# Optimization experiments

Hardware: AMD Instinct MI355X
Metric: run time of the kernel (lower is better)

The kernel has to match this reference:

```python
import jax, jax.numpy as jnp
import numpy as np

B, S, NH, D_IN = 64, 512, 4, 256   # batch, seq_len, rnn n_head, input_dim
H = 256                            # hidden_dim == attention activation_dim
AH = 256                           # attention_hidden_dim (attn out_dim)
OUT = 3                            # output_dim (sentiment classes)


def setup_inputs() -> dict:
    key = jax.random.key(0)
    ks = jax.random.split(key, 9)
    def p(k, shape, scale=0.05):
        return jax.random.normal(k, shape, dtype=jnp.float32) * scale
    return dict(
        x=jax.random.normal(ks[0], (B, S, NH, D_IN), dtype=jnp.float32),
        Wk=p(ks[1], (D_IN, H)), bk=jnp.zeros((H,), jnp.float32),
        Wq=p(ks[2], (H, H)),    bq=jnp.zeros((H,), jnp.float32),
        w_mlp=p(ks[3], (2 * H,)),
        Wproj=p(ks[4], (H, AH)), bproj=jnp.zeros((AH,), jnp.float32),
        W1=p(ks[5], (D_IN + AH, H)), b1=jnp.zeros((H,), jnp.float32),
        W2=p(ks[6], (H, H)),    b2=jnp.zeros((H,), jnp.float32),
        Wo=p(ks[7], (NH * H, OUT)), bo=jnp.zeros((OUT,), jnp.float32),
    )


def _cell(x_t, hidden, params):
    Wk, bk, Wq, bq, w_mlp, Wproj, bproj, W1, b1, W2, b2, Wo, bo = params
    kx = x_t @ Wk + bk           # [B, NH, H]  keys from step input
    qx = hidden @ Wq + bq        # [B, NH, H]  queries from hidden state
    w1, w2 = w_mlp[:H], w_mlp[H:]
    # MLP score: s[b,i,j] = tanh(cat(kx[b,j], qx[b,i]) . w) = tanh(kx[b,j].w1 + qx[b,i].w2)
    score = jnp.tanh((qx @ w2)[:, :, None] + (kx @ w1)[:, None, :])  # [B, NH, NH]
    score = jax.nn.softmax(score, axis=-1)
    attn = jnp.einsum('bij,bjh->bih', score, kx) @ Wproj + bproj     # [B, NH, AH]
    concat = jnp.concatenate([x_t, attn], axis=-1)                   # [B, NH, D_IN+AH]
    hidden_new = jax.nn.relu(concat @ W1 + b1) @ W2 + b2             # [B, NH, H]
    logits = hidden_new.reshape(B, NH * H) @ Wo + bo                 # [B, OUT]
    out = jax.nn.log_softmax(logits, axis=-1)
    return out, hidden_new


def reference(x, Wk, bk, Wq, bq, w_mlp, Wproj, bproj, W1, b1, W2, b2, Wo, bo):
    params = (Wk, bk, Wq, bq, w_mlp, Wproj, bproj, W1, b1, W2, b2, Wo, bo)
    h0 = jnp.zeros((B, NH, H), x.dtype)
    xs = jnp.swapaxes(x, 0, 1)  # [S, B, NH, D_IN] for scan over time
    def step(h, x_t):
        out, h_new = _cell(x_t, h, params)
        return h_new, out
    h_final, outs = jax.lax.scan(step, h0, xs)
    # return_sequence=False: last-step log-softmax output and final hidden
    return outs[-1], h_final
```

## Files before the change

kernel.cpp:

```cpp
#include <hip/hip_runtime.h>
#include <hip/hip_bf16.h>
#include <math.h>

#define BB   64
#define SS   512
#define NHH  4
#define DD   256
#define HH   256
#define LDH  264

typedef __attribute__((ext_vector_type(8))) short  short8;
typedef __attribute__((ext_vector_type(4))) float  floatx4;


__device__ __forceinline__ unsigned short f2b(float f) {
  __hip_bfloat16 h = __float2bfloat16(f);
  return __builtin_bit_cast(unsigned short, h);
}
__device__ __forceinline__ float b2f(unsigned short u) {
  unsigned v = (unsigned)u << 16;
  return __builtin_bit_cast(float, v);
}

__global__ __launch_bounds__(256) void init1_kernel(
    const float* __restrict__ Wk, const float* __restrict__ Wproj,
    const float* __restrict__ W1, const float* __restrict__ Wq,
    const float* __restrict__ bq, const float* __restrict__ w_mlp,
    const float* __restrict__ W2, const float* __restrict__ b2,
    const float* __restrict__ bk,
    float* __restrict__ ws, unsigned short* __restrict__ wpack)
{
  __shared__ float vsh[256];
  __shared__ float red[256];
  int tid = threadIdx.x;
  int b = blockIdx.x;

  if (b == 0) {
    const float* w2 = w_mlp + HH;
    {
      float a = 0.f;
      const float4* Wq4 = (const float4*)(Wq + tid * 256);
      const float4* w24 = (const float4*)w2;
      for (int k = 0; k < 64; ++k) {
        float4 wv = Wq4[k], xv = w24[k];
        a = fmaf(wv.x, xv.x, fmaf(wv.y, xv.y, fmaf(wv.z, xv.z, fmaf(wv.w, xv.w, a))));
      }
      vsh[tid] = a;
    }
    __syncthreads();
    {
      float a2 = 0.f;
      const float4* W24 = (const float4*)(W2 + tid * 256);
      const float4* v4  = (const float4*)vsh;
      for (int k = 0; k < 64; ++k) {
        float4 wv = W24[k], xv = v4[k];
        a2 = fmaf(wv.x, xv.x, fmaf(wv.y, xv.y, fmaf(wv.z, xv.z, fmaf(wv.w, xv.w, a2))));
      }
      ws[tid] = 2.f * a2;
    }
    red[tid] = bq[tid] * w_mlp[HH + tid];
    __syncthreads();
    for (int s = 128; s; s >>= 1) { if (tid < s) red[tid] += red[tid + s]; __syncthreads(); }
    float c = red[0];
    __syncthreads();
    ws[768 + tid] = 2.f * c;
    red[tid] = b2[tid] * vsh[tid];
    __syncthreads();
    for (int s = 128; s; s >>= 1) { if (tid < s) red[tid] += red[tid + s]; __syncthreads(); }
    if (tid == 0) ws[512] = 2.f * (red[0] + c);
    __syncthreads();
    red[tid] = bk[tid] * w_mlp[tid];
    __syncthreads();
    for (int s = 128; s; s >>= 1) { if (tid < s) red[tid] += red[tid + s]; __syncthreads(); }
    if (tid == 0) ws[513] = 2.f * red[0];
    return;
  }

  if (b <= 256) {
    int idx = (b - 1) * 256 + tid;
    int j    = idx & 7;
    int lane = (idx >> 3) & 63;
    int ks   = (idx >> 9) & 7;
    int pan  = idx >> 12;
    int k = ks * 32 + ((lane >> 4) << 3) + j;
    int n = pan * 16 + (lane & 15);
    wpack[idx] = f2b(W1[k * 256 + n]);
    return;
  }

  {
    int r = b - 257;
    const float* w1b = W1 + 256 * 256;
    float acc = 0.f;
    for (int k = 0; k < 256; ++k)
      acc = fmaf(Wproj[r * 256 + k], w1b[k * 256 + tid], acc);
    ws[132096 + r * 256 + tid] = acc;
  }
}

__global__ __launch_bounds__(256) void init2_kernel(
    const float* __restrict__ Wk, const float* __restrict__ W1,
    const float* __restrict__ bproj, const float* __restrict__ bk,
    const float* __restrict__ w_mlp, const float* __restrict__ b1,
    float* __restrict__ ws, unsigned short* __restrict__ wpack)
{
  __shared__ float red[256];
  int tid = threadIdx.x;
  int b = blockIdx.x;
  const float* Wc = ws + 132096;

  if (b < 256) {
    int r = b;
    float acc = 0.f;
    for (int k = 0; k < 256; ++k)
      acc = fmaf(Wk[r * 256 + k], Wc[k * 256 + tid], acc);
    int n = tid;
    int pan = n >> 4, ks = r >> 5, j = r & 7;
    int lane = ((r >> 3) & 3) * 16 + (n & 15);
    wpack[65536 + pan * 4096 + ks * 512 + lane * 8 + j] = f2b(acc);
    red[tid] = Wk[r * 256 + tid] * w_mlp[tid];
    __syncthreads();
    for (int s = 128; s; s >>= 1) { if (tid < s) red[tid] += red[tid + s]; __syncthreads(); }
    if (tid == 0) ws[197632 + r] = 2.f * red[0];
    return;
  }

  {
    const float* w1b = W1 + 256 * 256;
    float a3 = 0.f;
    for (int k = 0; k < 256; ++k)
      a3 = fmaf(bproj[k], w1b[k * 256 + tid], a3);
    for (int k = 0; k < 256; ++k)
      a3 = fmaf(bk[k], Wc[k * 256 + tid], a3);
    ws[256 + tid] = a3;
    ws[197888 + tid] = a3 + b1[tid];
  }
}

__device__ __forceinline__ void mfma_gemm4(
    const unsigned short* A_lds, const short8* __restrict__ Bp,
    const float* __restrict__ bias, floatx4 acc[4][4], int l, int w)
{
  int col = l & 15, quad = l >> 4;
#pragma unroll
  for (int pp = 0; pp < 4; ++pp) {
    float bv = bias ? bias[(w * 4 + pp) * 16 + col] : 0.f;
#pragma unroll
    for (int mf = 0; mf < 4; ++mf)
      acc[mf][pp] = (floatx4){bv, bv, bv, bv};
  }
  const short8* Bb = Bp + (size_t)(w * 4) * 512 + l;
  short8 bb[3][4];
  short8 aa[2][4];
#pragma unroll
  for (int pp = 0; pp < 4; ++pp) bb[0][pp] = Bb[pp * 512];
#pragma unroll
  for (int pp = 0; pp < 4; ++pp) bb[1][pp] = Bb[pp * 512 + 64];
#pragma unroll
  for (int mf = 0; mf < 4; ++mf)
    aa[0][mf] = *(const short8*)(A_lds + (mf * 16 + col) * LDH + quad * 8);
#pragma unroll
  for (int kb = 0; kb < 8; ++kb) {
    if (kb + 2 < 8) {
#pragma unroll
      for (int pp = 0; pp < 4; ++pp)
        bb[(kb + 2) % 3][pp] = Bb[pp * 512 + (kb + 2) * 64];
    }
    if (kb + 1 < 8) {
#pragma unroll
      for (int mf = 0; mf < 4; ++mf)
        aa[(kb + 1) & 1][mf] =
            *(const short8*)(A_lds + (mf * 16 + col) * LDH + (kb + 1) * 32 + quad * 8);
    }
#pragma unroll
    for (int mf = 0; mf < 4; ++mf)
#pragma unroll
      for (int pp = 0; pp < 4; ++pp)
        acc[mf][pp] = __builtin_amdgcn_mfma_f32_16x16x32_bf16(
            aa[kb & 1][mf], bb[kb % 3][pp], acc[mf][pp], 0, 0, 0);
  }
}

__device__ __forceinline__ void acc_to_global_f32(
    float* __restrict__ dst, const floatx4 acc[4][4],
    int l, int w, int b, int tt)
{
  int col = l & 15, quad = l >> 4;
#pragma unroll
  for (int mf = 0; mf < 4; ++mf)
#pragma unroll
    for (int r = 0; r < 4; ++r) {
      int m2 = mf * 16 + quad * 4 + r;
      size_t base = (((size_t)(tt * 16 + (m2 >> 2)) * 64 + b) * 4 + (m2 & 3)) * 256;
#pragma unroll
      for (int pp = 0; pp < 4; ++pp)
        dst[base + (w * 4 + pp) * 16 + col] = acc[mf][pp][r];
    }
}

__device__ void precompute_block(
    int px, const float* __restrict__ x, const unsigned short* __restrict__ wpack,
    const float* __restrict__ ws,
    float* __restrict__ kw_c, float* __restrict__ xw1_c,
    float* __restrict__ kpw_c, int t0, char* smem)
{
  float* kwbuf = (float*)smem;
  unsigned short* XS = (unsigned short*)(smem + 2048);

  int b  = px & 63;
  int tt = px >> 6;
  int tid = threadIdx.x;
  int l = tid & 63, w = tid >> 6;

  const float4* xsrc = (const float4*)(x + (size_t)(b * SS + t0 + tt * 16) * NHH * DD);
#pragma unroll
  for (int i = 0; i < 16; ++i) {
    int f4 = i * 256 + tid;
    int r = f4 >> 6, c4 = f4 & 63;
    float4 v = xsrc[f4];
    ushort4 h;
    h.x = f2b(v.x); h.y = f2b(v.y); h.z = f2b(v.z); h.w = f2b(v.w);
    *(ushort4*)&XS[r * LDH + c4 * 4] = h;
  }
  __syncthreads();

  const short8* wpA = (const short8*)(wpack);
  const short8* wpD = (const short8*)(wpack + 65536);

  {
    const float* wkw = ws + 197632;
    float part = 0.f;
    const unsigned short* trow = XS + l * LDH + w * 64;
#pragma unroll
    for (int j8 = 0; j8 < 8; ++j8) {
      short8 tv = *(const short8*)(trow + j8 * 8);
#pragma unroll
      for (int j = 0; j < 8; ++j)
        part = fmaf(b2f((unsigned short)tv[j]), wkw[w * 64 + j8 * 8 + j], part);
    }
    kwbuf[l * 4 + w] = part;
  }

  floatx4 acc[4][4];

  mfma_gemm4(XS, wpA, ws + 197888, acc, l, w);
  acc_to_global_f32(xw1_c, acc, l, w, b, tt);

  mfma_gemm4(XS, wpD, nullptr, acc, l, w);
  acc_to_global_f32(kpw_c, acc, l, w, b, tt);

  __syncthreads();
  if (tid < 64) {
    float s = kwbuf[tid * 4] + kwbuf[tid * 4 + 1] + kwbuf[tid * 4 + 2] + kwbuf[tid * 4 + 3]
            + ws[513];
    kw_c[((size_t)(tt * 16 + (tid >> 2)) * 64 + b) * 4 + (tid & 3)] = s;
  }
}

__device__ __forceinline__ float wave_reduce_sum(float x) {
#define DPPSTEP(ctrl, rmask)                                                   \
  {                                                                            \
    int _s = __builtin_amdgcn_update_dpp(0, __builtin_bit_cast(int, x),        \
                                         (ctrl), (rmask), 0xf, true);          \
    x += __builtin_bit_cast(float, _s);                                        \
  }
  DPPSTEP(0x111, 0xf)
  DPPSTEP(0x112, 0xf)
  DPPSTEP(0x114, 0xf)
  DPPSTEP(0x118, 0xf)
  DPPSTEP(0x142, 0xa)
  DPPSTEP(0x143, 0xc)
#undef DPPSTEP
  return __builtin_bit_cast(float, __builtin_amdgcn_readlane(__builtin_bit_cast(int, x), 63));
}

__device__ void seq_block(
    const float* __restrict__ xw1_c, const float* __restrict__ kpw_c,
    const float* __restrict__ kw_c, float* __restrict__ ws,
    float* __restrict__ relu_u, int t0, int n)
{
  int b = blockIdx.x;
  int tid = threadIdx.x;
  int i = tid >> 6, l = tid & 63;

  float4 v2v = ((const float4*)ws)[l];
  float c2s = ws[512];
  float qw2 = ws[768 + b * 4 + i];

  struct Slot { float4 x, k0, k1, k2, k3, kw; };
  struct SP { const float4 *xp, *kp, *kw; };

  const float4* xw4 = (const float4*)xw1_c;
  const float4* kp4 = (const float4*)kpw_c;
  const float4* kw4 = (const float4*)kw_c;

  SP p0 = { xw4 + (b * 4 + i) * 64 + l,             kp4 + b * 256 + l,             kw4 + b };
  SP p1 = { p0.xp + 16384, p0.kp + 16384, p0.kw + 64 };
  SP p2 = { p1.xp + 16384, p1.kp + 16384, p1.kw + 64 };
  SP p3 = { p2.xp + 16384, p2.kp + 16384, p2.kw + 64 };

  auto refill = [&](Slot& s, SP& p) {
    s.x  = *p.xp;
    s.k0 = p.kp[0];
    s.k1 = p.kp[64];
    s.k2 = p.kp[128];
    s.k3 = p.kp[192];
    s.kw = *p.kw;
    p.xp += 65536; p.kp += 65536; p.kw += 256;
  };

  auto step = [&](Slot& s, int t) {
    float r0 = __builtin_amdgcn_rcpf(__expf(qw2 + s.kw.x) + 1.f);
    float r1 = __builtin_amdgcn_rcpf(__expf(qw2 + s.kw.y) + 1.f);
    float r2 = __builtin_amdgcn_rcpf(__expf(qw2 + s.kw.z) + 1.f);
    float r3 = __builtin_amdgcn_rcpf(__expf(qw2 + s.kw.w) + 1.f);
    float q0 = __expf(fmaf(-2.f, r0, 1.f));
    float q1 = __expf(fmaf(-2.f, r1, 1.f));
    float q2 = __expf(fmaf(-2.f, r2, 1.f));
    float q3 = __expf(fmaf(-2.f, r3, 1.f));
    float inv = __builtin_amdgcn_rcpf((q0 + q1) + (q2 + q3));
    float4 a;
    a.x = fmaf(q0, s.k0.x, fmaf(q1, s.k1.x, fmaf(q2, s.k2.x, q3 * s.k3.x)));
    a.y = fmaf(q0, s.k0.y, fmaf(q1, s.k1.y, fmaf(q2, s.k2.y, q3 * s.k3.y)));
    a.z = fmaf(q0, s.k0.z, fmaf(q1, s.k1.z, fmaf(q2, s.k2.z, q3 * s.k3.z)));
    a.w = fmaf(q0, s.k0.w, fmaf(q1, s.k1.w, fmaf(q2, s.k2.w, q3 * s.k3.w)));
    float4 u;
    u.x = fmaf(a.x, inv, s.x.x); u.y = fmaf(a.y, inv, s.x.y);
    u.z = fmaf(a.z, inv, s.x.z); u.w = fmaf(a.w, inv, s.x.w);
    float4 rr;
    rr.x = fmaxf(u.x, 0.f); rr.y = fmaxf(u.y, 0.f);
    rr.z = fmaxf(u.z, 0.f); rr.w = fmaxf(u.w, 0.f);
    float d = fmaf(rr.x, v2v.x, rr.y * v2v.y) + fmaf(rr.z, v2v.z, rr.w * v2v.w);
    qw2 = wave_reduce_sum(d) + c2s;
    if (t0 + t == SS - 1)
      *(float4*)&relu_u[(size_t)(b * 4 + i) * 256 + l * 4] = rr;
  };

  Slot s0, s1, s2, s3;
  refill(s0, p0); refill(s1, p1); refill(s2, p2); refill(s3, p3);
  for (int t = 0; t < n; t += 4) {
    step(s0, t);     refill(s0, p0);
    step(s1, t + 1); refill(s1, p1);
    step(s2, t + 2); refill(s2, p2);
    step(s3, t + 3); refill(s3, p3);
  }
  if (l == 0) ws[768 + b * 4 + i] = qw2;
}

__global__ __launch_bounds__(256, 1) void fused_kernel(
    const float* __restrict__ x, const unsigned short* __restrict__ wpack,
    float* kwB, float* xw1B, float* kpwB, int t0_pre,
    const float* kwA, const float* xw1A, const float* kpwA,
    int t0_seq, int n_seq,
    float* __restrict__ ws, float* __restrict__ relu_u)
{
  __shared__ __align__(16) char smem[2048 + 64 * LDH * 2];
  if (blockIdx.x < 64) {
    if (n_seq > 0) seq_block(xw1A, kpwA, kwA, ws, relu_u, t0_seq, n_seq);
    return;
  }
  precompute_block(blockIdx.x - 64, x, wpack, ws,
                   kwB, xw1B, kpwB, t0_pre, smem);
}

__global__ __launch_bounds__(256) void final_hidden_kernel(
    const float* __restrict__ relu_u, const float* __restrict__ W2,
    const float* __restrict__ b2, float* __restrict__ out)
{
  __shared__ float rs[256];
  int row = blockIdx.x;
  int tid = threadIdx.x;
  rs[tid] = relu_u[(size_t)row * 256 + tid];
  __syncthreads();
  float acc = b2[tid];
  for (int k = 0; k < 256; ++k) acc = fmaf(rs[k], W2[k * 256 + tid], acc);
  out[192 + (size_t)row * 256 + tid] = acc;
}

__global__ __launch_bounds__(256) void final_logits_kernel(
    const float* __restrict__ hf, const float* __restrict__ Wo,
    const float* __restrict__ bo, float* __restrict__ outp)
{
  __shared__ float r0[256], r1[256], r2[256];
  int b = blockIdx.x;
  int tid = threadIdx.x;
  float a0 = 0.f, a1 = 0.f, a2 = 0.f;
  for (int k = tid; k < 1024; k += 256) {
    float h = hf[(size_t)b * 1024 + k];
    a0 = fmaf(h, Wo[k * 3 + 0], a0);
    a1 = fmaf(h, Wo[k * 3 + 1], a1);
    a2 = fmaf(h, Wo[k * 3 + 2], a2);
  }
  r0[tid] = a0; r1[tid] = a1; r2[tid] = a2;
  __syncthreads();
  for (int s = 128; s; s >>= 1) {
    if (tid < s) { r0[tid] += r0[tid + s]; r1[tid] += r1[tid + s]; r2[tid] += r2[tid + s]; }
    __syncthreads();
  }
  if (tid == 0) {
    float l0 = r0[0] + bo[0], l1 = r1[0] + bo[1], l2 = r2[0] + bo[2];
    float m = fmaxf(l0, fmaxf(l1, l2));
    float lse = m + logf(expf(l0 - m) + expf(l1 - m) + expf(l2 - m));
    outp[b * 3 + 0] = l0 - lse;
    outp[b * 3 + 1] = l1 - lse;
    outp[b * 3 + 2] = l2 - lse;
  }
}

extern "C" void kernel_launch(void* const* d_in, const int* in_sizes, int n_in,
                              void* d_out, int out_size, void* d_ws, size_t ws_size,
                              hipStream_t stream)
{
  const float* x     = (const float*)d_in[0];
  const float* Wk    = (const float*)d_in[1];
  const float* bk    = (const float*)d_in[2];
  const float* Wq    = (const float*)d_in[3];
  const float* bq    = (const float*)d_in[4];
  const float* w_mlp = (const float*)d_in[5];
  const float* Wproj = (const float*)d_in[6];
  const float* bproj = (const float*)d_in[7];
  const float* W1    = (const float*)d_in[8];
  const float* b1    = (const float*)d_in[9];
  const float* W2    = (const float*)d_in[10];
  const float* b2    = (const float*)d_in[11];
  const float* Wo    = (const float*)d_in[12];
  const float* bo    = (const float*)d_in[13];
  float* out = (float*)d_out;
  float* ws  = (float*)d_ws;

  float* ru = ws + 1024;
  unsigned short* wpack = (unsigned short*)(ws + 66560);
  const size_t OFF_CH = 198144;
  const long per_t = 256 + 2 * 65536;

  long ws_floats = (long)(ws_size / 4);
  long avail = ws_floats - (long)OFF_CH - 8L * per_t;

  int Tc = 128;
  while (Tc > 0 && 2L * Tc * per_t > avail) Tc -= 16;
  bool pipelined = (Tc >= 16);
  if (!pipelined) {
    Tc = 128;
    while (Tc > 16 && (long)Tc * per_t > avail) Tc -= 16;
  }

  float* bufA = ws + OFF_CH;
  float* bufB = pipelined ? bufA + (size_t)Tc * per_t : bufA;

  auto kw_of  = [&](float* base) { return base; };
  auto xw_of  = [&](float* base) { return base + (size_t)Tc * 256; };
  auto kpw_of = [&](float* base) { return base + (size_t)Tc * 256 + (size_t)Tc * 65536; };

  init1_kernel<<<513, 256, 0, stream>>>(Wk, Wproj, W1, Wq, bq, w_mlp, W2, b2, bk,
                                        ws, wpack);
  init2_kernel<<<257, 256, 0, stream>>>(Wk, W1, bproj, bk, w_mlp, b1, ws, wpack);

  int C = (SS + Tc - 1) / Tc;

  if (pipelined) {
    for (int r = 0; r <= C; ++r) {
      bool hasPre = (r < C);
      bool hasSeq = (r >= 1);
      int t0p = r * Tc;
      int np  = hasPre ? ((SS - t0p) < Tc ? (SS - t0p) : Tc) : 0;
      int t0s = (r - 1) * Tc;
      int ns  = hasSeq ? ((SS - t0s) < Tc ? (SS - t0s) : Tc) : 0;
      float* pB = ((r & 1) ? bufB : bufA);
      float* pA = (((r - 1) & 1) ? bufB : bufA);
      int grid = 64 + (hasPre ? 64 * (np / 16) : 0);
      fused_kernel<<<grid, 256, 0, stream>>>(
          x, wpack,
          kw_of(pB), xw_of(pB), kpw_of(pB), t0p,
          kw_of(pA), xw_of(pA), kpw_of(pA), t0s, ns,
          ws, ru);
    }
  } else {
    for (int c = 0; c < C; ++c) {
      int t0 = c * Tc;
      int n = (SS - t0) < Tc ? (SS - t0) : Tc;
      fused_kernel<<<64 + 64 * (n / 16), 256, 0, stream>>>(
          x, wpack,
          kw_of(bufA), xw_of(bufA), kpw_of(bufA), t0,
          kw_of(bufA), xw_of(bufA), kpw_of(bufA), 0, 0,
          ws, ru);
      fused_kernel<<<64, 256, 0, stream>>>(
          x, wpack,
          kw_of(bufA), xw_of(bufA), kpw_of(bufA), t0,
          kw_of(bufA), xw_of(bufA), kpw_of(bufA), t0, n,
          ws, ru);
    }
  }

  final_hidden_kernel<<<BB * NHH, 256, 0, stream>>>(ru, W2, b2, out);
  final_logits_kernel<<<BB, 256, 0, stream>>>(out + 192, Wo, bo, out);
}
```

Before: 412.1 us.

## Replace chunked launches with single persistent producer-consumer kernel using flags

Replaces the per-chunk sequence of fused kernel launches with one launch. In it, 2048 producer blocks compute the precomputed projections for all timesteps and publish per-(batch, tile) ready flags, while 256 consumer blocks (one wavefront each, per batch and head) spin on those flags and run the recurrence. Intermediate xw1/kpw buffers are now stored as bf16 instead of fp32, halving their traffic. Launch bounds change to allow two blocks per CU. This removes launch gaps and chunk barriers, but it relies on consumer and producer blocks being co-resident, has a bounded-spin fallback that could silently read stale data, and loses some precision from the bf16 storage.

```diff
diff --git a/kernel.cpp b/kernel.cpp
--- a/kernel.cpp
+++ b/kernel.cpp
@@ -11,7 +11,12 @@
 
 typedef __attribute__((ext_vector_type(8))) short  short8;
 typedef __attribute__((ext_vector_type(4))) float  floatx4;
-
+typedef unsigned long long u64;
+
+#define OFF_FLAGS 198144
+#define OFF_KW    200192
+#define OFF_XW    332288
+#define OFF_KPW   (OFF_XW + 16908288)
 
 __device__ __forceinline__ unsigned short f2b(float f) {
   __hip_bfloat16 h = __float2bfloat16(f);
@@ -20,6 +25,10 @@
 __device__ __forceinline__ float b2f(unsigned short u) {
   unsigned v = (unsigned)u << 16;
   return __builtin_bit_cast(float, v);
+}
+
+__device__ __forceinline__ u64 cld(const u64* p) {
+  return __hip_atomic_load(p, __ATOMIC_RELAXED, __HIP_MEMORY_SCOPE_AGENT);
 }
 
 __global__ __launch_bounds__(256) void init1_kernel(
@@ -36,6 +45,10 @@
   int b = blockIdx.x;
 
   if (b == 0) {
+    int* flags = (int*)(ws + OFF_FLAGS);
+#pragma unroll
+    for (int k = 0; k < 8; ++k) flags[k * 256 + tid] = 0;
+
     const float* w2 = w_mlp + HH;
     {
       float a = 0.f;
@@ -181,8 +194,8 @@
   }
 }
 
-__device__ __forceinline__ void acc_to_global_f32(
-    float* __restrict__ dst, const floatx4 acc[4][4],
+__device__ __forceinline__ void acc_to_global(
+    unsigned short* __restrict__ dst, const floatx4 acc[4][4],
     int l, int w, int b, int tt)
 {
   int col = l & 15, quad = l >> 4;
@@ -194,15 +207,13 @@
       size_t base = (((size_t)(tt * 16 + (m2 >> 2)) * 64 + b) * 4 + (m2 & 3)) * 256;
 #pragma unroll
       for (int pp = 0; pp < 4; ++pp)
-        dst[base + (w * 4 + pp) * 16 + col] = acc[mf][pp][r];
-    }
-}
-
-__device__ void precompute_block(
+        dst[base + (w * 4 + pp) * 16 + col] = f2b(acc[mf][pp][r]);
+    }
+}
+
+__device__ void producer_block(
     int px, const float* __restrict__ x, const unsigned short* __restrict__ wpack,
-    const float* __restrict__ ws,
-    float* __restrict__ kw_c, float* __restrict__ xw1_c,
-    float* __restrict__ kpw_c, int t0, char* smem)
+    float* __restrict__ ws, char* smem)
 {
   float* kwbuf = (float*)smem;
   unsigned short* XS = (unsigned short*)(smem + 2048);
@@ -212,7 +223,12 @@
   int tid = threadIdx.x;
   int l = tid & 63, w = tid >> 6;
 
-  const float4* xsrc = (const float4*)(x + (size_t)(b * SS + t0 + tt * 16) * NHH * DD);
+  float* kw_c = ws + OFF_KW;
+  unsigned short* xw1_c = (unsigned short*)(ws + OFF_XW);
+  unsigned short* kpw_c = (unsigned short*)(ws + OFF_KPW);
+  int* flags = (int*)(ws + OFF_FLAGS);
+
+  const float4* xsrc = (const float4*)(x + (size_t)(b * SS + tt * 16) * NHH * DD);
 #pragma unroll
   for (int i = 0; i < 16; ++i) {
     int f4 = i * 256 + tid;
@@ -244,10 +260,10 @@
   floatx4 acc[4][4];
 
   mfma_gemm4(XS, wpA, ws + 197888, acc, l, w);
-  acc_to_global_f32(xw1_c, acc, l, w, b, tt);
+  acc_to_global(xw1_c, acc, l, w, b, tt);
 
   mfma_gemm4(XS, wpD, nullptr, acc, l, w);
-  acc_to_global_f32(kpw_c, acc, l, w, b, tt);
+  acc_to_global(kpw_c, acc, l, w, b, tt);
 
   __syncthreads();
   if (tid < 64) {
@@ -255,6 +271,12 @@
             + ws[513];
     kw_c[((size_t)(tt * 16 + (tid >> 2)) * 64 + b) * 4 + (tid & 3)] = s;
   }
+
+  __threadfence();
+  __syncthreads();
+  if (tid == 0)
+    __hip_atomic_store(&flags[b * 32 + tt], 1, __ATOMIC_RELEASE,
+                       __HIP_MEMORY_SCOPE_AGENT);
 }
 
 __device__ __forceinline__ float wave_reduce_sum(float x) {
@@ -274,39 +296,51 @@
   return __builtin_bit_cast(float, __builtin_amdgcn_readlane(__builtin_bit_cast(int, x), 63));
 }
 
-__device__ void seq_block(
-    const float* __restrict__ xw1_c, const float* __restrict__ kpw_c,
-    const float* __restrict__ kw_c, float* __restrict__ ws,
-    float* __restrict__ relu_u, int t0, int n)
-{
-  int b = blockIdx.x;
-  int tid = threadIdx.x;
-  int i = tid >> 6, l = tid & 63;
+__device__ void consumer_block(
+    int c, float* __restrict__ ws, float* __restrict__ relu_u)
+{
+  int tid = threadIdx.x;
+  if (tid >= 64) return;
+  int l = tid;
+  int b = c >> 2, i = c & 3;
 
   float4 v2v = ((const float4*)ws)[l];
   float c2s = ws[512];
   float qw2 = ws[768 + b * 4 + i];
 
-  struct Slot { float4 x, k0, k1, k2, k3, kw; };
-  struct SP { const float4 *xp, *kp, *kw; };
-
-  const float4* xw4 = (const float4*)xw1_c;
-  const float4* kp4 = (const float4*)kpw_c;
-  const float4* kw4 = (const float4*)kw_c;
-
-  SP p0 = { xw4 + (b * 4 + i) * 64 + l,             kp4 + b * 256 + l,             kw4 + b };
-  SP p1 = { p0.xp + 16384, p0.kp + 16384, p0.kw + 64 };
-  SP p2 = { p1.xp + 16384, p1.kp + 16384, p1.kw + 64 };
-  SP p3 = { p2.xp + 16384, p2.kp + 16384, p2.kw + 64 };
+  const u64* xw8 = (const u64*)(ws + OFF_XW);
+  const u64* kp8 = (const u64*)(ws + OFF_KPW);
+  const u64* kw8 = (const u64*)(ws + OFF_KW);
+  const int* flags = (const int*)(ws + OFF_FLAGS) + b * 32;
+
+  struct Slot { ushort4 x, k0, k1, k2, k3; float4 kw; };
+  struct SP { const u64 *xp, *kp, *kw; };
+
+  SP p0 = { xw8 + (b * 4 + i) * 64 + l, kp8 + b * 256 + l, kw8 + b * 2 };
+  SP p1 = { p0.xp + 16384, p0.kp + 16384, p0.kw + 128 };
+  SP p2 = { p1.xp + 16384, p1.kp + 16384, p1.kw + 128 };
+  SP p3 = { p2.xp + 16384, p2.kp + 16384, p2.kw + 128 };
+
+  auto waitf = [&](int tt) {
+    const int* fp = flags + tt;
+    int spins = 0;
+    while (__hip_atomic_load(fp, __ATOMIC_RELAXED, __HIP_MEMORY_SCOPE_AGENT) == 0) {
+      __builtin_amdgcn_s_sleep(8);
+      if (++spins > (1 << 20)) break;
+    }
+    __asm__ volatile("" ::: "memory");
+  };
 
   auto refill = [&](Slot& s, SP& p) {
-    s.x  = *p.xp;
-    s.k0 = p.kp[0];
-    s.k1 = p.kp[64];
-    s.k2 = p.kp[128];
-    s.k3 = p.kp[192];
-    s.kw = *p.kw;
-    p.xp += 65536; p.kp += 65536; p.kw += 256;
+    s.x  = __builtin_bit_cast(ushort4, cld(p.xp));
+    s.k0 = __builtin_bit_cast(ushort4, cld(p.kp));
+    s.k1 = __builtin_bit_cast(ushort4, cld(p.kp + 64));
+    s.k2 = __builtin_bit_cast(ushort4, cld(p.kp + 128));
+    s.k3 = __builtin_bit_cast(ushort4, cld(p.kp + 192));
+    float2 kl = __builtin_bit_cast(float2, cld(p.kw));
+    float2 kh = __builtin_bit_cast(float2, cld(p.kw + 1));
+    s.kw = (float4){kl.x, kl.y, kh.x, kh.y};
+    p.xp += 65536; p.kp += 65536; p.kw += 512;
   };
 
   auto step = [&](Slot& s, int t) {
@@ -319,48 +353,55 @@
     float q2 = __expf(fmaf(-2.f, r2, 1.f));
     float q3 = __expf(fmaf(-2.f, r3, 1.f));
     float inv = __builtin_amdgcn_rcpf((q0 + q1) + (q2 + q3));
+    float4 K0 = {b2f(s.k0.x), b2f(s.k0.y), b2f(s.k0.z), b2f(s.k0.w)};
+    float4 K1 = {b2f(s.k1.x), b2f(s.k1.y), b2f(s.k1.z), b2f(s.k1.w)};
+    float4 K2 = {b2f(s.k2.x), b2f(s.k2.y), b2f(s.k2.z), b2f(s.k2.w)};
+    float4 K3 = {b2f(s.k3.x), b2f(s.k3.y), b2f(s.k3.z), b2f(s.k3.w)};
+    float4 X  = {b2f(s.x.x), b2f(s.x.y), b2f(s.x.z), b2f(s.x.w)};
     float4 a;
-    a.x = fmaf(q0, s.k0.x, fmaf(q1, s.k1.x, fmaf(q2, s.k2.x, q3 * s.k3.x)));
-    a.y = fmaf(q0, s.k0.y, fmaf(q1, s.k1.y, fmaf(q2, s.k2.y, q3 * s.k3.y)));
-    a.z = fmaf(q0, s.k0.z, fmaf(q1, s.k1.z, fmaf(q2, s.k2.z, q3 * s.k3.z)));
-    a.w = fmaf(q0, s.k0.w, fmaf(q1, s.k1.w, fmaf(q2, s.k2.w, q3 * s.k3.w)));
+    a.x = fmaf(q0, K0.x, fmaf(q1, K1.x, fmaf(q2, K2.x, q3 * K3.x)));
+    a.y = fmaf(q0, K0.y, fmaf(q1, K1.y, fmaf(q2, K2.y, q3 * K3.y)));
+    a.z = fmaf(q0, K0.z, fmaf(q1, K1.z, fmaf(q2, K2.z, q3 * K3.z)));
+    a.w = fmaf(q0, K0.w, fmaf(q1, K1.w, fmaf(q2, K2.w, q3 * K3.w)));
     float4 u;
-    u.x = fmaf(a.x, inv, s.x.x); u.y = fmaf(a.y, inv, s.x.y);
-    u.z = fmaf(a.z, inv, s.x.z); u.w = fmaf(a.w, inv, s.x.w);
+    u.x = fmaf(a.x, inv, X.x); u.y = fmaf(a.y, inv, X.y);
+    u.z = fmaf(a.z, inv, X.z); u.w = fmaf(a.w, inv, X.w);
     float4 rr;
     rr.x = fmaxf(u.x, 0.f); rr.y = fmaxf(u.y, 0.f);
     rr.z = fmaxf(u.z, 0.f); rr.w = fmaxf(u.w, 0.f);
     float d = fmaf(rr.x, v2v.x, rr.y * v2v.y) + fmaf(rr.z, v2v.z, rr.w * v2v.w);
     qw2 = wave_reduce_sum(d) + c2s;
-    if (t0 + t == SS - 1)
+    if (t == SS - 1)
       *(float4*)&relu_u[(size_t)(b * 4 + i) * 256 + l * 4] = rr;
   };
 
   Slot s0, s1, s2, s3;
+  waitf(0);
   refill(s0, p0); refill(s1, p1); refill(s2, p2); refill(s3, p3);
-  for (int t = 0; t < n; t += 4) {
-    step(s0, t);     refill(s0, p0);
-    step(s1, t + 1); refill(s1, p1);
-    step(s2, t + 2); refill(s2, p2);
-    step(s3, t + 3); refill(s3, p3);
-  }
-  if (l == 0) ws[768 + b * 4 + i] = qw2;
-}
-
-__global__ __launch_bounds__(256, 1) void fused_kernel(
+  for (int tt = 0; tt < 32; ++tt) {
+    waitf(tt < 31 ? tt + 1 : 31);
+    int t = tt * 16;
+#pragma unroll 4
+    for (int g = 0; g < 4; ++g) {
+      step(s0, t);     refill(s0, p0);
+      step(s1, t + 1); refill(s1, p1);
+      step(s2, t + 2); refill(s2, p2);
+      step(s3, t + 3); refill(s3, p3);
+      t += 4;
+    }
+  }
+}
+
+__global__ __launch_bounds__(256, 2) void fused_kernel(
     const float* __restrict__ x, const unsigned short* __restrict__ wpack,
-    float* kwB, float* xw1B, float* kpwB, int t0_pre,
-    const float* kwA, const float* xw1A, const float* kpwA,
-    int t0_seq, int n_seq,
     float* __restrict__ ws, float* __restrict__ relu_u)
 {
   __shared__ __align__(16) char smem[2048 + 64 * LDH * 2];
-  if (blockIdx.x < 64) {
-    if (n_seq > 0) seq_block(xw1A, kpwA, kwA, ws, relu_u, t0_seq, n_seq);
+  if (blockIdx.x < 256) {
+    consumer_block(blockIdx.x, ws, relu_u);
     return;
   }
-  precompute_block(blockIdx.x - 64, x, wpack, ws,
-                   kwB, xw1B, kpwB, t0_pre, smem);
+  producer_block(blockIdx.x - 256, x, wpack, ws, smem);
 }
 
 __global__ __launch_bounds__(256) void final_hidden_kernel(
@@ -430,66 +471,12 @@
 
   float* ru = ws + 1024;
   unsigned short* wpack = (unsigned short*)(ws + 66560);
-  const size_t OFF_CH = 198144;
-  const long per_t = 256 + 2 * 65536;
-
-  long ws_floats = (long)(ws_size / 4);
-  long avail = ws_floats - (long)OFF_CH - 8L * per_t;
-
-  int Tc = 128;
-  while (Tc > 0 && 2L * Tc * per_t > avail) Tc -= 16;
-  bool pipelined = (Tc >= 16);
-  if (!pipelined) {
-    Tc = 128;
-    while (Tc > 16 && (long)Tc * per_t > avail) Tc -= 16;
-  }
-
-  float* bufA = ws + OFF_CH;
-  float* bufB = pipelined ? bufA + (size_t)Tc * per_t : bufA;
-
-  auto kw_of  = [&](float* base) { return base; };
-  auto xw_of  = [&](float* base) { return base + (size_t)Tc * 256; };
-  auto kpw_of = [&](float* base) { return base + (size_t)Tc * 256 + (size_t)Tc * 65536; };
 
   init1_kernel<<<513, 256, 0, stream>>>(Wk, Wproj, W1, Wq, bq, w_mlp, W2, b2, bk,
                                         ws, wpack);
   init2_kernel<<<257, 256, 0, stream>>>(Wk, W1, bproj, bk, w_mlp, b1, ws, wpack);
 
-  int C = (SS + Tc - 1) / Tc;
-
-  if (pipelined) {
-    for (int r = 0; r <= C; ++r) {
-      bool hasPre = (r < C);
-      bool hasSeq = (r >= 1);
-      int t0p = r * Tc;
-      int np  = hasPre ? ((SS - t0p) < Tc ? (SS - t0p) : Tc) : 0;
-      int t0s = (r - 1) * Tc;
-      int ns  = hasSeq ? ((SS - t0s) < Tc ? (SS - t0s) : Tc) : 0;
-      float* pB = ((r & 1) ? bufB : bufA);
-      float* pA = (((r - 1) & 1) ? bufB : bufA);
-      int grid = 64 + (hasPre ? 64 * (np / 16) : 0);
-      fused_kernel<<<grid, 256, 0, stream>>>(
-          x, wpack,
-          kw_of(pB), xw_of(pB), kpw_of(pB), t0p,
-          kw_of(pA), xw_of(pA), kpw_of(pA), t0s, ns,
-          ws, ru);
-    }
-  } else {
-    for (int c = 0; c < C; ++c) {
-      int t0 = c * Tc;
-      int n = (SS - t0) < Tc ? (SS - t0) : Tc;
-      fused_kernel<<<64 + 64 * (n / 16), 256, 0, stream>>>(
-          x, wpack,
-          kw_of(bufA), xw_of(bufA), kpw_of(bufA), t0,
-          kw_of(bufA), xw_of(bufA), kpw_of(bufA), 0, 0,
-          ws, ru);
-      fused_kernel<<<64, 256, 0, stream>>>(
-          x, wpack,
-          kw_of(bufA), xw_of(bufA), kpw_of(bufA), t0,
-          kw_of(bufA), xw_of(bufA), kpw_of(bufA), t0, n,
-          ws, ru);
-    }
-  }
+  fused_kernel<<<256 + 2048, 256, 0, stream>>>(x, wpack, ws, ru);
 
   final_hidden_kernel<<<BB * NHH, 256, 0, stream>>>(ru, W2, b2, out);
   final_logits_kernel<<<BB, 256, 0, stream>>>(out + 192, Wo, bo, out);
```

After: 827.4 us. 101% more time.
